# Optimization experiments

Measured on AMD Instinct MI355X. Metric: run time of the kernel, lower is better.

The kernel has to match this reference:

```python
import jax, jax.numpy as jnp
import numpy as np

N_FEATURES = 256
N_LAYERS = 256  # MZI layers; 2*N_LAYERS PSBS sublayers
BATCH = 1024


def _make_indexAB(nF):
    A = np.array([[2 * k, 2 * k + 1] for k in range(nF // 2)], np.int32)
    B = [[2 * k + 1, 2 * k + 2] for k in range((nF - 1) // 2)]
    while len(B) < nF // 2:
        B.append([-1, -1])  # padding sentinel, masked out
    return A, np.array(B, np.int32)


def _make_index(nF, nLayers):
    A, B = _make_indexAB(nF)
    blocks = ([A] * 2 + [B] * 2) * (nLayers // 2)
    if nLayers % 2 == 1:
        blocks += [A] * 2
    return np.stack(blocks).astype(np.int32)  # [2*nLayers, nF//2, 2]


def setup_inputs() -> dict:
    key = jax.random.key(0)
    k1, k2, k3 = jax.random.split(key, 3)
    nSub = 2 * N_LAYERS
    nAng = N_FEATURES // 2
    index = jnp.asarray(_make_index(N_FEATURES, N_LAYERS))
    return {
        "x_real": jax.random.normal(k1, (BATCH, N_FEATURES), jnp.float32),
        "x_imag": jax.random.normal(k2, (BATCH, N_FEATURES), jnp.float32),
        "params": jax.random.normal(k3, (nSub, nAng), jnp.float32),  # torch.randn init
        "ps_params": jnp.zeros((N_FEATURES,), jnp.float32),  # ModulePS zeros init
        "index": index,
        "split": jnp.zeros((nSub, nAng), jnp.float32),  # buffer, default zeros
        "atten": jnp.ones((nSub, N_FEATURES), jnp.float32),  # buffer, default ones
    }


def _psbs_mesh(x, params, i_safe, j_safe, valid, split, atten):
    # x: [B, F] complex64. Each sublayer: phase e^{i theta} on top port, then
    # beamsplitter [[cos a, i sin a],[i sin a, cos a]] with a = pi/4 + split,
    # then per-feature diagonal attenuation.
    def step(x, xs):
        theta, isf, jsf, vld, sp, at = xs
        xu = x[:, isf]  # [B, A]
        xv = x[:, jsf]
        u = xu * jnp.exp(1j * theta)[None, :]
        ang = jnp.float32(np.pi / 4) + sp
        t = jnp.cos(ang)
        r = jnp.sin(ang)
        yu = t * u + 1j * r * xv
        yv = 1j * r * u + t * xv
        zero = jnp.zeros((), x.dtype)
        # scatter deltas; invalid (padded) pairs add 0 so duplicate dummy index 0 is safe
        x = x.at[:, isf].add(jnp.where(vld, yu - xu, zero))
        x = x.at[:, jsf].add(jnp.where(vld, yv - xv, zero))
        return x * at[None, :], None

    x, _ = jax.lax.scan(step, x, (params, i_safe, j_safe, valid, split, atten))
    return x


def reference(x_real, x_imag, params, ps_params, index, split, atten):
    x = (x_real + 1j * x_imag).astype(jnp.complex64)
    i_idx = index[:, :, 0]
    j_idx = index[:, :, 1]
    valid = i_idx >= 0
    i_safe = jnp.where(valid, i_idx, 0)
    j_safe = jnp.where(valid, j_idx, 0)
    x = _psbs_mesh(x, params, i_safe, j_safe, valid, split, atten)
    # final diagonal phase shift (ModulePS)
    return x * jnp.exp(1j * ps_params)[None, :]
```

## Files before the change

kernel.cpp:

```cpp
#include <hip/hip_runtime.h>
#include <math.h>

#define NF    256
#define NSUB  512
#define NB    1024
#define NITER 128
#define PI4   0.78539816339744830962f

#define PS_OFF   (NITER * 1024)
#define FLAG_OFF (PS_OFF + 512)
#define WS_REQ   ((size_t)(FLAG_OFF + 1) * sizeof(float))

__device__ __forceinline__ bool looks_zero(const void* p) {
  const unsigned* u = (const unsigned*)p;
  return (u[1] | u[25] | u[111]) == 0u;
}
__device__ __forceinline__ bool looks_ones(const void* p) {
  const unsigned* u = (const unsigned*)p;
  return u[1] == 0x3F800000u && u[3] == 0x3F800000u && u[257] == 0x3F800000u;
}

__global__ void flag_init_kernel(float* ws) {
  ((unsigned*)ws)[FLAG_OFF] = 0u;
}

__global__ __launch_bounds__(256) void check_kernel(
    const void* __restrict__ pp0, const void* __restrict__ pp1,
    const void* __restrict__ pi0, const void* __restrict__ pi1,
    float* __restrict__ ws) {
  const unsigned* split = (const unsigned*)(looks_zero(pp0) ? pp0 : pp1);
  const unsigned* atten = (const unsigned*)(looks_ones(pi0) ? pi0 : pi1);
  const int i = blockIdx.x * 256 + threadIdx.x;
  unsigned bad = 0u;
  if (atten[i] != 0x3F800000u) bad = 1u;
  if (i < 65536 && split[i] != 0u) bad = 1u;
  if (bad) atomicOr(((unsigned*)ws) + FLAG_OFF, 1u);
}

__global__ __launch_bounds__(256) void precompute3_kernel(
    const void* __restrict__ pp0, const void* __restrict__ pp1,
    const float* __restrict__ psp, float* __restrict__ ws) {
  const float* params = looks_zero(pp0) ? (const float*)pp1 : (const float*)pp0;
  const int t = blockIdx.x;
  const int j = threadIdx.x;
  if (t == NITER) {
    float sn, cs;
    sincosf(psp[j], &sn, &cs);
    ((float2*)(ws + PS_OFF))[j] = make_float2(cs, sn);
    return;
  }
  float e1r, e1i, fr, fi;
  int k, ln;
  if (j < 128) {
    float s1, c1, s2, c2;
    sincosf(params[(size_t)(4 * t) * 128 + j], &s1, &c1);
    sincosf(params[(size_t)(4 * t + 1) * 128 + j], &s2, &c2);
    e1r = 0.5f * c1; e1i = 0.5f * s1;
    fr = 0.5f * (c2 + 1.f); fi = 0.5f * s2;
    k = j & 1; ln = j >> 1;
  } else {
    const int m = j - 128;
    if (m < 127) {
      float s1, c1, s2, c2;
      sincosf(params[(size_t)(4 * t + 2) * 128 + m], &s1, &c1);
      sincosf(params[(size_t)(4 * t + 3) * 128 + m], &s2, &c2);
      e1r = 0.5f * c1; e1i = 0.5f * s1;
      fr = 0.5f * (c2 + 1.f); fi = 0.5f * s2;
    } else {
      e1r = -0.5f; e1i = 0.f; fr = 0.f; fi = 0.f;
    }
    k = 2 + (m & 1); ln = m >> 1;
  }
  ((float4*)ws)[t * 256 + k * 64 + ln] = make_float4(e1r, e1i, fr, fi);
}

__device__ __forceinline__ void applyC(float& ur, float& ui, float& vr, float& vi,
                                       const float4 K) {
  const float wr = K.x * ur - K.y * ui;
  const float wi = K.x * ui + K.y * ur;
  const float e2r = 2.f * K.z - 1.f;
  const float e2i = 2.f * K.w;
  const float zr = e2r * wr - e2i * wi;
  const float zi = e2r * wi + e2i * wr;
  const float gr = K.z * vr - K.w * vi;
  const float gi = K.z * vi + K.w * vr;
  const float nur = (zr - wr) - gi;
  const float nui = (zi - wi) + gr;
  const float nvr = (vr - gr) - (zi + wi);
  const float nvi = (vi - gi) + (zr + wr);
  ur = nur; ui = nui; vr = nvr; vi = nvi;
}

__device__ __forceinline__ void mzi(float& ur, float& ui, float& vr, float& vi,
                                    const float4 k) {
  const float c = k.x, s = k.y, t = k.z, r = k.w;
  const float pr  = c * ur - s * ui;
  const float pi_ = s * ur + c * ui;
  const float nur = t * pr  - r * vi;
  const float nui = t * pi_ + r * vr;
  const float nvr = t * vr - r * pi_;
  const float nvi = t * vi + r * pr;
  ur = nur; ui = nui; vr = nvr; vi = nvi;
}
struct Coef { float4 a, b, c; };
__device__ __forceinline__ Coef makeCoefRaw(const float* params, const float* split,
                                            const float* atten, int s, int lane) {
  Coef k;
  const float2 th = *(const float2*)(params + (size_t)s * 128 + 2 * lane);
  const float2 sp = *(const float2*)(split + (size_t)s * 128 + 2 * lane);
  k.c = *(const float4*)(atten + (size_t)s * NF + 4 * lane);
  float sn, cs, rr, tt;
  sincosf(th.x, &sn, &cs);
  sincosf(PI4 + sp.x, &rr, &tt);
  k.a = make_float4(cs, sn, tt, rr);
  sincosf(th.y, &sn, &cs);
  sincosf(PI4 + sp.y, &rr, &tt);
  k.b = make_float4(cs, sn, tt, rr);
  return k;
}

#define ITER_BODY(C0, C1, C2, C3)                                          \
  {                                                                        \
    applyC(x0r, x0i, x1r, x1i, C0);                                        \
    applyC(x2r, x2i, x3r, x3i, C1);                                        \
    const float s0r = x0r, s0i = x0i;                                      \
    const float d3r = __shfl_down(x0r, 1), d3i = __shfl_down(x0i, 1);      \
    x0r = x1r; x0i = x1i; x1r = x2r; x1i = x2i; x2r = x3r; x2i = x3i;      \
    x3r = d3r; x3i = d3i;                                                  \
    applyC(x0r, x0i, x1r, x1i, C2);                                        \
    applyC(x2r, x2i, x3r, x3i, C3);                                        \
    const float u0r = __shfl_up(x3r, 1), u0i = __shfl_up(x3i, 1);          \
    x3r = x2r; x3i = x2i; x2r = x1r; x2i = x1i; x1r = x0r; x1i = x0i;      \
    x0r = lane ? u0r : s0r;                                                \
    x0i = lane ? u0i : s0i;                                                \
  }

__global__ __launch_bounds__(256) void mesh3_kernel(
    const float* __restrict__ xr_in, const float* __restrict__ xi_in,
    const float* __restrict__ ws,
    const void* __restrict__ pp0, const void* __restrict__ pp1,
    const void* __restrict__ pi0, const void* __restrict__ pi1,
    const float* __restrict__ psp,
    float* __restrict__ out) {
  const int lane = threadIdx.x & 63;
  const int wv   = threadIdx.x >> 6;
  const int row  = blockIdx.x * 4 + wv;

  const float4 r4 = ((const float4*)(xr_in + (size_t)row * NF))[lane];
  const float4 i4 = ((const float4*)(xi_in + (size_t)row * NF))[lane];
  float x0r = r4.x, x1r = r4.y, x2r = r4.z, x3r = r4.w;
  float x0i = i4.x, x1i = i4.y, x2i = i4.z, x3i = i4.w;

  const unsigned flag = ((const unsigned*)ws)[FLAG_OFF];
  if (flag == 0u) {
    const float4* cb = (const float4*)ws + lane;
    float4 A0 = cb[0],   A1 = cb[64],  A2 = cb[128], A3 = cb[192];
    float4 B0 = cb[256], B1 = cb[320], B2 = cb[384], B3 = cb[448];
#pragma unroll 1
    for (int tt = 0; tt < 64; ++tt) {
      const int pa = (tt < 63) ? (2 * tt + 2) * 256 : 0;
      const float4 nA0 = cb[pa], nA1 = cb[pa + 64], nA2 = cb[pa + 128], nA3 = cb[pa + 192];
      ITER_BODY(A0, A1, A2, A3);
      A0 = nA0; A1 = nA1; A2 = nA2; A3 = nA3;
      const int pb = (tt < 63) ? (2 * tt + 3) * 256 : 256;
      const float4 nB0 = cb[pb], nB1 = cb[pb + 64], nB2 = cb[pb + 128], nB3 = cb[pb + 192];
      ITER_BODY(B0, B1, B2, B3);
      B0 = nB0; B1 = nB1; B2 = nB2; B3 = nB3;
    }
    const float2* psc = (const float2*)(ws + PS_OFF);
    const float2 p0 = psc[4 * lane + 0];
    const float2 p1 = psc[4 * lane + 1];
    const float2 p2 = psc[4 * lane + 2];
    const float2 p3 = psc[4 * lane + 3];
    const float o0r = x0r * p0.x - x0i * p0.y, o0i = x0r * p0.y + x0i * p0.x;
    const float o1r = x1r * p1.x - x1i * p1.y, o1i = x1r * p1.y + x1i * p1.x;
    const float o2r = x2r * p2.x - x2i * p2.y, o2i = x2r * p2.y + x2i * p2.x;
    const float o3r = x3r * p3.x - x3i * p3.y, o3i = x3r * p3.y + x3i * p3.x;
    float4* op = (float4*)out;
    const size_t base = (size_t)row * 64 + lane;
    op[base] = make_float4(o0r, o1r, o2r, o3r);
    op[(size_t)NB * 64 + base] = make_float4(o0i, o1i, o2i, o3i);
    return;
  }

  {
    const float* params = looks_zero(pp0) ? (const float*)pp1 : (const float*)pp0;
    const float* split  = looks_zero(pp0) ? (const float*)pp0 : (const float*)pp1;
    const float* atten  = looks_ones(pi0) ? (const float*)pi0 : (const float*)pi1;
#pragma unroll 1
    for (int s = 0; s < NSUB; s += 4) {
      {
        Coef k = makeCoefRaw(params, split, atten, s, lane);
        mzi(x0r, x0i, x1r, x1i, k.a);
        mzi(x2r, x2i, x3r, x3i, k.b);
        x0r *= k.c.x; x0i *= k.c.x; x1r *= k.c.y; x1i *= k.c.y;
        x2r *= k.c.z; x2i *= k.c.z; x3r *= k.c.w; x3i *= k.c.w;
      }
      {
        Coef k = makeCoefRaw(params, split, atten, s + 1, lane);
        mzi(x0r, x0i, x1r, x1i, k.a);
        mzi(x2r, x2i, x3r, x3i, k.b);
        x0r *= k.c.x; x0i *= k.c.x; x1r *= k.c.y; x1i *= k.c.y;
        x2r *= k.c.z; x2i *= k.c.z; x3r *= k.c.w; x3i *= k.c.w;
      }
#pragma unroll
      for (int q = 2; q < 4; ++q) {
        Coef k = makeCoefRaw(params, split, atten, s + q, lane);
        mzi(x1r, x1i, x2r, x2i, k.a);
        const float nvr = __shfl_down(x0r, 1);
        const float nvi = __shfl_down(x0i, 1);
        const float c = k.b.x, sv = k.b.y, t = k.b.z, r = k.b.w;
        const float pr  = c * x3r - sv * x3i;
        const float pi_ = sv * x3r + c * x3i;
        const float yur = t * pr  - r * nvi;
        const float yui = t * pi_ + r * nvr;
        const float yvr = t * nvr - r * pi_;
        const float yvi = t * nvi + r * pr;
        const float svr = __shfl_up(yvr, 1);
        const float svi = __shfl_up(yvi, 1);
        if (lane < 63) { x3r = yur; x3i = yui; }
        if (lane > 0)  { x0r = svr; x0i = svi; }
        x0r *= k.c.x; x0i *= k.c.x; x1r *= k.c.y; x1i *= k.c.y;
        x2r *= k.c.z; x2i *= k.c.z; x3r *= k.c.w; x3i *= k.c.w;
      }
    }
    float c0, s0, c1, s1, c2, s2, c3, s3;
    sincosf(psp[4 * lane + 0], &s0, &c0);
    sincosf(psp[4 * lane + 1], &s1, &c1);
    sincosf(psp[4 * lane + 2], &s2, &c2);
    sincosf(psp[4 * lane + 3], &s3, &c3);
    const float o0r = x0r * c0 - x0i * s0, o0i = x0r * s0 + x0i * c0;
    const float o1r = x1r * c1 - x1i * s1, o1i = x1r * s1 + x1i * c1;
    const float o2r = x2r * c2 - x2i * s2, o2i = x2r * s2 + x2i * c2;
    const float o3r = x3r * c3 - x3i * s3, o3i = x3r * s3 + x3i * c3;
    float4* op = (float4*)out;
    const size_t base = (size_t)row * 64 + lane;
    op[base] = make_float4(o0r, o1r, o2r, o3r);
    op[(size_t)NB * 64 + base] = make_float4(o0i, o1i, o2i, o3i);
  }
}

__global__ __launch_bounds__(256) void mesh_raw_kernel(
    const float* __restrict__ xr_in, const float* __restrict__ xi_in,
    const void* __restrict__ pp0, const void* __restrict__ pp1,
    const void* __restrict__ pi0, const void* __restrict__ pi1,
    const float* __restrict__ psp, float* __restrict__ out) {
  const int lane = threadIdx.x & 63;
  const int wv   = threadIdx.x >> 6;
  const int row  = blockIdx.x * 4 + wv;
  const float4 r4 = ((const float4*)(xr_in + (size_t)row * NF))[lane];
  const float4 i4 = ((const float4*)(xi_in + (size_t)row * NF))[lane];
  float x0r = r4.x, x1r = r4.y, x2r = r4.z, x3r = r4.w;
  float x0i = i4.x, x1i = i4.y, x2i = i4.z, x3i = i4.w;
  const float* params = looks_zero(pp0) ? (const float*)pp1 : (const float*)pp0;
  const float* split  = looks_zero(pp0) ? (const float*)pp0 : (const float*)pp1;
  const float* atten  = looks_ones(pi0) ? (const float*)pi0 : (const float*)pi1;
#pragma unroll 1
  for (int s = 0; s < NSUB; s += 4) {
    for (int q = 0; q < 2; ++q) {
      Coef k = makeCoefRaw(params, split, atten, s + q, lane);
      mzi(x0r, x0i, x1r, x1i, k.a);
      mzi(x2r, x2i, x3r, x3i, k.b);
      x0r *= k.c.x; x0i *= k.c.x; x1r *= k.c.y; x1i *= k.c.y;
      x2r *= k.c.z; x2i *= k.c.z; x3r *= k.c.w; x3i *= k.c.w;
    }
    for (int q = 2; q < 4; ++q) {
      Coef k = makeCoefRaw(params, split, atten, s + q, lane);
      mzi(x1r, x1i, x2r, x2i, k.a);
      const float nvr = __shfl_down(x0r, 1);
      const float nvi = __shfl_down(x0i, 1);
      const float c = k.b.x, sv = k.b.y, t = k.b.z, r = k.b.w;
      const float pr  = c * x3r - sv * x3i;
      const float pi_ = sv * x3r + c * x3i;
      const float yur = t * pr  - r * nvi;
      const float yui = t * pi_ + r * nvr;
      const float yvr = t * nvr - r * pi_;
      const float yvi = t * nvi + r * pr;
      const float svr = __shfl_up(yvr, 1);
      const float svi = __shfl_up(yvi, 1);
      if (lane < 63) { x3r = yur; x3i = yui; }
      if (lane > 0)  { x0r = svr; x0i = svi; }
      x0r *= k.c.x; x0i *= k.c.x; x1r *= k.c.y; x1i *= k.c.y;
      x2r *= k.c.z; x2i *= k.c.z; x3r *= k.c.w; x3i *= k.c.w;
    }
  }
  float c0, s0, c1, s1, c2, s2, c3, s3;
  sincosf(psp[4 * lane + 0], &s0, &c0);
  sincosf(psp[4 * lane + 1], &s1, &c1);
  sincosf(psp[4 * lane + 2], &s2, &c2);
  sincosf(psp[4 * lane + 3], &s3, &c3);
  const float o0r = x0r * c0 - x0i * s0, o0i = x0r * s0 + x0i * c0;
  const float o1r = x1r * c1 - x1i * s1, o1i = x1r * s1 + x1i * c1;
  const float o2r = x2r * c2 - x2i * s2, o2i = x2r * s2 + x2i * c2;
  const float o3r = x3r * c3 - x3i * s3, o3i = x3r * s3 + x3i * c3;
  float4* op = (float4*)out;
  const size_t base = (size_t)row * 64 + lane;
  op[base] = make_float4(o0r, o1r, o2r, o3r);
  op[(size_t)NB * 64 + base] = make_float4(o0i, o1i, o2i, o3i);
}

extern "C" void kernel_launch(void* const* d_in, const int* in_sizes, int n_in,
                              void* d_out, int out_size, void* d_ws, size_t ws_size,
                              hipStream_t stream) {
  const void* px[2] = { d_in[0], d_in[1] };
  const void* pp[2] = { d_in[2], d_in[5] };
  const void* pi2[2] = { d_in[4], d_in[6] };
  const void* pps = d_in[3];
  {
    const void* sx[2]; const void* sp[2]; const void* si[2];
    const void* s256 = nullptr;
    int nx = 0, npp = 0, ni = 0;
    for (int i = 0; i < n_in; ++i) {
      const int sz = in_sizes[i];
      if (sz == 262144 && nx < 2)      sx[nx++] = d_in[i];
      else if (sz == 65536 && npp < 2) sp[npp++] = d_in[i];
      else if (sz == 131072 && ni < 2) si[ni++] = d_in[i];
      else if (sz == 256)              s256 = d_in[i];
    }
    if (nx == 2)  { px[0] = sx[0];  px[1] = sx[1]; }
    if (npp == 2) { pp[0] = sp[0];  pp[1] = sp[1]; }
    if (ni == 2)  { pi2[0] = si[0]; pi2[1] = si[1]; }
    if (s256)     pps = s256;
  }
  float* out = (float*)d_out;

  if (ws_size >= WS_REQ) {
    float* ws = (float*)d_ws;
    flag_init_kernel<<<1, 1, 0, stream>>>(ws);
    check_kernel<<<512, 256, 0, stream>>>(pp[0], pp[1], pi2[0], pi2[1], ws);
    precompute3_kernel<<<NITER + 1, 256, 0, stream>>>(pp[0], pp[1],
                                                      (const float*)pps, ws);
    mesh3_kernel<<<NB / 4, 256, 0, stream>>>(
        (const float*)px[0], (const float*)px[1], ws,
        pp[0], pp[1], pi2[0], pi2[1], (const float*)pps, out);
  } else {
    mesh_raw_kernel<<<NB / 4, 256, 0, stream>>>(
        (const float*)px[0], (const float*)px[1],
        pp[0], pp[1], pi2[0], pi2[1], (const float*)pps, out);
  }
}
```

Before: 64.87 us.

## Collapse groups of eight sublayers into banded 9-tap transfer kernels

Adds a precompute that multiplies every 8 consecutive PSBS sublayers into a banded 9-diagonal complex transfer matrix per output feature. The mesh kernel then applies 64 banded mat-vec steps using neighbour shuffles, instead of 512 sublayer updates. This cuts the serial dependency chain and the number of shuffles per row. In exchange it adds a memset, two precompute kernels and more coefficient loads per step, and the fallback raw path moves into a separate guarded kernel. The fast path still depends on the existing check that split is zero and atten is one.

```diff
diff --git a/kernel.cpp b/kernel.cpp
--- a/kernel.cpp
+++ b/kernel.cpp
@@ -5,11 +5,17 @@
 #define NSUB  512
 #define NB    1024
 #define NITER 128
+#define NGRP  64
 #define PI4   0.78539816339744830962f
+#define RS    0.70710678118654752440f
 
 #define PS_OFF   (NITER * 1024)
 #define FLAG_OFF (PS_OFF + 512)
-#define WS_REQ   ((size_t)(FLAG_OFF + 1) * sizeof(float))
+#define KB_OFF   131600
+#define KB_FLOATS (NGRP * 9 * 256 * 2)
+#define E_OFF    (KB_OFF + KB_FLOATS)
+#define WS1_REQ  ((size_t)(FLAG_OFF + 1) * sizeof(float))
+#define WS2_REQ  ((size_t)(E_OFF + NSUB * 128 * 2) * sizeof(float))
 
 __device__ __forceinline__ bool looks_zero(const void* p) {
   const unsigned* u = (const unsigned*)p;
@@ -74,6 +80,149 @@
   ((float4*)ws)[t * 256 + k * 64 + ln] = make_float4(e1r, e1i, fr, fi);
 }
 
+__global__ __launch_bounds__(128) void stage1_kernel(
+    const void* __restrict__ pp0, const void* __restrict__ pp1,
+    float* __restrict__ ws) {
+  const float* params = looks_zero(pp0) ? (const float*)pp1 : (const float*)pp0;
+  const int idx = blockIdx.x * 128 + threadIdx.x;
+  float sn, cs;
+  sincosf(params[idx], &sn, &cs);
+  ws[E_OFF + 2 * idx]     = cs;
+  ws[E_OFF + 2 * idx + 1] = sn;
+}
+
+__global__ __launch_bounds__(256) void stage2_kernel(float* __restrict__ ws) {
+  const int g = blockIdx.x;
+  const int j = threadIdx.x;
+  const float2* Et = (const float2*)(ws + E_OFF);
+  float wr[9], wi[9];
+#pragma unroll
+  for (int q = 0; q < 9; ++q) { wr[q] = 0.f; wi[q] = 0.f; }
+  wr[4] = 1.f;
+  const bool jeven = ((j & 1) == 0);
+
+#define FULLPAIR(SU)                                                        \
+  {                                                                         \
+    const int p = j - 4 + (SU);                                             \
+    const bool ok = isA ? (p >= 0 && p <= 254) : (p >= 1 && p <= 253);      \
+    if (ok) {                                                               \
+      const float2 E = Et[s * 128 + (isA ? (p >> 1) : ((p - 1) >> 1))];     \
+      const float ur = wr[SU], ui = wi[SU];                                 \
+      const float vr = wr[(SU) + 1], vi = wi[(SU) + 1];                     \
+      const float er = E.x * ur - E.y * ui;                                 \
+      const float ei = E.x * ui + E.y * ur;                                 \
+      wr[SU] = (er - vi) * RS;       wi[SU] = (ei + vr) * RS;               \
+      wr[(SU) + 1] = (vr - ei) * RS; wi[(SU) + 1] = (vi + er) * RS;         \
+    }                                                                       \
+  }
+#define HALFU8                                                              \
+  {                                                                         \
+    const int p = j + 4;                                                    \
+    const bool ok = isA ? (p >= 0 && p <= 254) : (p >= 1 && p <= 253);      \
+    if (ok) {                                                               \
+      const float2 E = Et[s * 128 + (isA ? (p >> 1) : ((p - 1) >> 1))];     \
+      const float er = E.x * wr[8] - E.y * wi[8];                           \
+      const float ei = E.x * wi[8] + E.y * wr[8];                           \
+      wr[8] = er * RS; wi[8] = ei * RS;                                     \
+    }                                                                       \
+  }
+#define HALFV0                                                              \
+  {                                                                         \
+    const int p = j - 5;                                                    \
+    const bool ok = isA ? (p >= 0) : (p >= 1);                              \
+    if (ok) { wr[0] *= RS; wi[0] *= RS; }                                   \
+  }
+
+#pragma unroll
+  for (int ss = 0; ss < 8; ++ss) {
+    const int s = 8 * g + ss;
+    const bool isA = ((ss & 2) == 0);
+    const bool pat0 = (jeven == isA);
+    if (pat0) {
+      FULLPAIR(0) FULLPAIR(2) FULLPAIR(4) FULLPAIR(6) HALFU8
+    } else {
+      FULLPAIR(1) FULLPAIR(3) FULLPAIR(5) FULLPAIR(7) HALFV0
+    }
+  }
+#undef FULLPAIR
+#undef HALFU8
+#undef HALFV0
+
+#pragma unroll
+  for (int slot = 0; slot < 9; ++slot) {
+    const int f = j - 4 + slot;
+    if (f >= 0 && f < 256) {
+      const size_t o = KB_OFF + (((size_t)g * 9 + (8 - slot)) * 256 + f) * 2;
+      ws[o]     = wr[slot];
+      ws[o + 1] = wi[slot];
+    }
+  }
+}
+
+__global__ __launch_bounds__(256) void mesh6_kernel(
+    const float* __restrict__ xr_in, const float* __restrict__ xi_in,
+    const float* __restrict__ ws, float* __restrict__ out) {
+  if (((const unsigned*)ws)[FLAG_OFF] != 0u) return;
+  const int lane = threadIdx.x & 63;
+  const int wv   = threadIdx.x >> 6;
+  const int row  = blockIdx.x * 4 + wv;
+
+  const float4 r4 = ((const float4*)(xr_in + (size_t)row * NF))[lane];
+  const float4 i4 = ((const float4*)(xi_in + (size_t)row * NF))[lane];
+  float x0r = r4.x, x1r = r4.y, x2r = r4.z, x3r = r4.w;
+  float x0i = i4.x, x1i = i4.y, x2i = i4.z, x3i = i4.w;
+
+  const float* kb = ws + KB_OFF + 8 * lane;
+
+#pragma unroll 1
+  for (int g = 0; g < NGRP; ++g) {
+    float xwr[12], xwi[12];
+    xwr[0] = __shfl_up(x0r, 1);  xwi[0] = __shfl_up(x0i, 1);
+    xwr[1] = __shfl_up(x1r, 1);  xwi[1] = __shfl_up(x1i, 1);
+    xwr[2] = __shfl_up(x2r, 1);  xwi[2] = __shfl_up(x2i, 1);
+    xwr[3] = __shfl_up(x3r, 1);  xwi[3] = __shfl_up(x3i, 1);
+    xwr[4] = x0r; xwi[4] = x0i;  xwr[5] = x1r; xwi[5] = x1i;
+    xwr[6] = x2r; xwi[6] = x2i;  xwr[7] = x3r; xwi[7] = x3i;
+    xwr[8]  = __shfl_down(x0r, 1); xwi[8]  = __shfl_down(x0i, 1);
+    xwr[9]  = __shfl_down(x1r, 1); xwi[9]  = __shfl_down(x1i, 1);
+    xwr[10] = __shfl_down(x2r, 1); xwi[10] = __shfl_down(x2i, 1);
+    xwr[11] = __shfl_down(x3r, 1); xwi[11] = __shfl_down(x3i, 1);
+
+    float ar0 = 0.f, ai0 = 0.f, ar1 = 0.f, ai1 = 0.f;
+    float ar2 = 0.f, ai2 = 0.f, ar3 = 0.f, ai3 = 0.f;
+    const float* kg = kb + (size_t)g * 4608;
+#pragma unroll
+    for (int dd = 0; dd < 9; ++dd) {
+      const float4 ka = *(const float4*)(kg + dd * 512);
+      const float4 kc = *(const float4*)(kg + dd * 512 + 4);
+      ar0 = fmaf(ka.x, xwr[dd], ar0);     ar0 = fmaf(-ka.y, xwi[dd], ar0);
+      ai0 = fmaf(ka.x, xwi[dd], ai0);     ai0 = fmaf(ka.y, xwr[dd], ai0);
+      ar1 = fmaf(ka.z, xwr[dd + 1], ar1); ar1 = fmaf(-ka.w, xwi[dd + 1], ar1);
+      ai1 = fmaf(ka.z, xwi[dd + 1], ai1); ai1 = fmaf(ka.w, xwr[dd + 1], ai1);
+      ar2 = fmaf(kc.x, xwr[dd + 2], ar2); ar2 = fmaf(-kc.y, xwi[dd + 2], ar2);
+      ai2 = fmaf(kc.x, xwi[dd + 2], ai2); ai2 = fmaf(kc.y, xwr[dd + 2], ai2);
+      ar3 = fmaf(kc.z, xwr[dd + 3], ar3); ar3 = fmaf(-kc.w, xwi[dd + 3], ar3);
+      ai3 = fmaf(kc.z, xwi[dd + 3], ai3); ai3 = fmaf(kc.w, xwr[dd + 3], ai3);
+    }
+    x0r = ar0; x0i = ai0; x1r = ar1; x1i = ai1;
+    x2r = ar2; x2i = ai2; x3r = ar3; x3i = ai3;
+  }
+
+  const float2* psc = (const float2*)(ws + PS_OFF);
+  const float2 p0 = psc[4 * lane + 0];
+  const float2 p1 = psc[4 * lane + 1];
+  const float2 p2 = psc[4 * lane + 2];
+  const float2 p3 = psc[4 * lane + 3];
+  const float o0r = x0r * p0.x - x0i * p0.y, o0i = x0r * p0.y + x0i * p0.x;
+  const float o1r = x1r * p1.x - x1i * p1.y, o1i = x1r * p1.y + x1i * p1.x;
+  const float o2r = x2r * p2.x - x2i * p2.y, o2i = x2r * p2.y + x2i * p2.x;
+  const float o3r = x3r * p3.x - x3i * p3.y, o3i = x3r * p3.y + x3i * p3.x;
+  float4* op = (float4*)out;
+  const size_t base = (size_t)row * 64 + lane;
+  op[base] = make_float4(o0r, o1r, o2r, o3r);
+  op[(size_t)NB * 64 + base] = make_float4(o0i, o1i, o2i, o3i);
+}
+
 __device__ __forceinline__ void applyC(float& ur, float& ui, float& vr, float& vi,
                                        const float4 K) {
   const float wr = K.x * ur - K.y * ui;
@@ -91,6 +240,62 @@
   ur = nur; ui = nui; vr = nvr; vi = nvi;
 }
 
+#define ITER_BODY(C0, C1, C2, C3)                                          \
+  {                                                                        \
+    applyC(x0r, x0i, x1r, x1i, C0);                                        \
+    applyC(x2r, x2i, x3r, x3i, C1);                                        \
+    const float s0r = x0r, s0i = x0i;                                      \
+    const float d3r = __shfl_down(x0r, 1), d3i = __shfl_down(x0i, 1);      \
+    x0r = x1r; x0i = x1i; x1r = x2r; x1i = x2i; x2r = x3r; x2i = x3i;      \
+    x3r = d3r; x3i = d3i;                                                  \
+    applyC(x0r, x0i, x1r, x1i, C2);                                        \
+    applyC(x2r, x2i, x3r, x3i, C3);                                        \
+    const float u0r = __shfl_up(x3r, 1), u0i = __shfl_up(x3i, 1);          \
+    x3r = x2r; x3i = x2i; x2r = x1r; x2i = x1i; x1r = x0r; x1i = x0i;      \
+    x0r = lane ? u0r : s0r;                                                \
+    x0i = lane ? u0i : s0i;                                                \
+  }
+
+__global__ __launch_bounds__(256) void mesh3_kernel(
+    const float* __restrict__ xr_in, const float* __restrict__ xi_in,
+    const float* __restrict__ ws, float* __restrict__ out) {
+  if (((const unsigned*)ws)[FLAG_OFF] != 0u) return;
+  const int lane = threadIdx.x & 63;
+  const int wv   = threadIdx.x >> 6;
+  const int row  = blockIdx.x * 4 + wv;
+  const float4 r4 = ((const float4*)(xr_in + (size_t)row * NF))[lane];
+  const float4 i4 = ((const float4*)(xi_in + (size_t)row * NF))[lane];
+  float x0r = r4.x, x1r = r4.y, x2r = r4.z, x3r = r4.w;
+  float x0i = i4.x, x1i = i4.y, x2i = i4.z, x3i = i4.w;
+  const float4* cb = (const float4*)ws + lane;
+  float4 A0 = cb[0],   A1 = cb[64],  A2 = cb[128], A3 = cb[192];
+  float4 B0 = cb[256], B1 = cb[320], B2 = cb[384], B3 = cb[448];
+#pragma unroll 1
+  for (int tt = 0; tt < 64; ++tt) {
+    const int pa = (tt < 63) ? (2 * tt + 2) * 256 : 0;
+    const float4 nA0 = cb[pa], nA1 = cb[pa + 64], nA2 = cb[pa + 128], nA3 = cb[pa + 192];
+    ITER_BODY(A0, A1, A2, A3);
+    A0 = nA0; A1 = nA1; A2 = nA2; A3 = nA3;
+    const int pb = (tt < 63) ? (2 * tt + 3) * 256 : 256;
+    const float4 nB0 = cb[pb], nB1 = cb[pb + 64], nB2 = cb[pb + 128], nB3 = cb[pb + 192];
+    ITER_BODY(B0, B1, B2, B3);
+    B0 = nB0; B1 = nB1; B2 = nB2; B3 = nB3;
+  }
+  const float2* psc = (const float2*)(ws + PS_OFF);
+  const float2 p0 = psc[4 * lane + 0];
+  const float2 p1 = psc[4 * lane + 1];
+  const float2 p2 = psc[4 * lane + 2];
+  const float2 p3 = psc[4 * lane + 3];
+  const float o0r = x0r * p0.x - x0i * p0.y, o0i = x0r * p0.y + x0i * p0.x;
+  const float o1r = x1r * p1.x - x1i * p1.y, o1i = x1r * p1.y + x1i * p1.x;
+  const float o2r = x2r * p2.x - x2i * p2.y, o2i = x2r * p2.y + x2i * p2.x;
+  const float o3r = x3r * p3.x - x3i * p3.y, o3i = x3r * p3.y + x3i * p3.x;
+  float4* op = (float4*)out;
+  const size_t base = (size_t)row * 64 + lane;
+  op[base] = make_float4(o0r, o1r, o2r, o3r);
+  op[(size_t)NB * 64 + base] = make_float4(o0i, o1i, o2i, o3i);
+}
+
 __device__ __forceinline__ void mzi(float& ur, float& ui, float& vr, float& vi,
                                     const float4 k) {
   const float c = k.x, s = k.y, t = k.z, r = k.w;
@@ -119,132 +324,14 @@
   return k;
 }
 
-#define ITER_BODY(C0, C1, C2, C3)                                          \
-  {                                                                        \
-    applyC(x0r, x0i, x1r, x1i, C0);                                        \
-    applyC(x2r, x2i, x3r, x3i, C1);                                        \
-    const float s0r = x0r, s0i = x0i;                                      \
-    const float d3r = __shfl_down(x0r, 1), d3i = __shfl_down(x0i, 1);      \
-    x0r = x1r; x0i = x1i; x1r = x2r; x1i = x2i; x2r = x3r; x2i = x3i;      \
-    x3r = d3r; x3i = d3i;                                                  \
-    applyC(x0r, x0i, x1r, x1i, C2);                                        \
-    applyC(x2r, x2i, x3r, x3i, C3);                                        \
-    const float u0r = __shfl_up(x3r, 1), u0i = __shfl_up(x3i, 1);          \
-    x3r = x2r; x3i = x2i; x2r = x1r; x2i = x1i; x1r = x0r; x1i = x0i;      \
-    x0r = lane ? u0r : s0r;                                                \
-    x0i = lane ? u0i : s0i;                                                \
-  }
-
-__global__ __launch_bounds__(256) void mesh3_kernel(
-    const float* __restrict__ xr_in, const float* __restrict__ xi_in,
-    const float* __restrict__ ws,
-    const void* __restrict__ pp0, const void* __restrict__ pp1,
-    const void* __restrict__ pi0, const void* __restrict__ pi1,
-    const float* __restrict__ psp,
-    float* __restrict__ out) {
-  const int lane = threadIdx.x & 63;
-  const int wv   = threadIdx.x >> 6;
-  const int row  = blockIdx.x * 4 + wv;
-
-  const float4 r4 = ((const float4*)(xr_in + (size_t)row * NF))[lane];
-  const float4 i4 = ((const float4*)(xi_in + (size_t)row * NF))[lane];
-  float x0r = r4.x, x1r = r4.y, x2r = r4.z, x3r = r4.w;
-  float x0i = i4.x, x1i = i4.y, x2i = i4.z, x3i = i4.w;
-
-  const unsigned flag = ((const unsigned*)ws)[FLAG_OFF];
-  if (flag == 0u) {
-    const float4* cb = (const float4*)ws + lane;
-    float4 A0 = cb[0],   A1 = cb[64],  A2 = cb[128], A3 = cb[192];
-    float4 B0 = cb[256], B1 = cb[320], B2 = cb[384], B3 = cb[448];
-#pragma unroll 1
-    for (int tt = 0; tt < 64; ++tt) {
-      const int pa = (tt < 63) ? (2 * tt + 2) * 256 : 0;
-      const float4 nA0 = cb[pa], nA1 = cb[pa + 64], nA2 = cb[pa + 128], nA3 = cb[pa + 192];
-      ITER_BODY(A0, A1, A2, A3);
-      A0 = nA0; A1 = nA1; A2 = nA2; A3 = nA3;
-      const int pb = (tt < 63) ? (2 * tt + 3) * 256 : 256;
-      const float4 nB0 = cb[pb], nB1 = cb[pb + 64], nB2 = cb[pb + 128], nB3 = cb[pb + 192];
-      ITER_BODY(B0, B1, B2, B3);
-      B0 = nB0; B1 = nB1; B2 = nB2; B3 = nB3;
-    }
-    const float2* psc = (const float2*)(ws + PS_OFF);
-    const float2 p0 = psc[4 * lane + 0];
-    const float2 p1 = psc[4 * lane + 1];
-    const float2 p2 = psc[4 * lane + 2];
-    const float2 p3 = psc[4 * lane + 3];
-    const float o0r = x0r * p0.x - x0i * p0.y, o0i = x0r * p0.y + x0i * p0.x;
-    const float o1r = x1r * p1.x - x1i * p1.y, o1i = x1r * p1.y + x1i * p1.x;
-    const float o2r = x2r * p2.x - x2i * p2.y, o2i = x2r * p2.y + x2i * p2.x;
-    const float o3r = x3r * p3.x - x3i * p3.y, o3i = x3r * p3.y + x3i * p3.x;
-    float4* op = (float4*)out;
-    const size_t base = (size_t)row * 64 + lane;
-    op[base] = make_float4(o0r, o1r, o2r, o3r);
-    op[(size_t)NB * 64 + base] = make_float4(o0i, o1i, o2i, o3i);
-    return;
-  }
-
-  {
-    const float* params = looks_zero(pp0) ? (const float*)pp1 : (const float*)pp0;
-    const float* split  = looks_zero(pp0) ? (const float*)pp0 : (const float*)pp1;
-    const float* atten  = looks_ones(pi0) ? (const float*)pi0 : (const float*)pi1;
-#pragma unroll 1
-    for (int s = 0; s < NSUB; s += 4) {
-      {
-        Coef k = makeCoefRaw(params, split, atten, s, lane);
-        mzi(x0r, x0i, x1r, x1i, k.a);
-        mzi(x2r, x2i, x3r, x3i, k.b);
-        x0r *= k.c.x; x0i *= k.c.x; x1r *= k.c.y; x1i *= k.c.y;
-        x2r *= k.c.z; x2i *= k.c.z; x3r *= k.c.w; x3i *= k.c.w;
-      }
-      {
-        Coef k = makeCoefRaw(params, split, atten, s + 1, lane);
-        mzi(x0r, x0i, x1r, x1i, k.a);
-        mzi(x2r, x2i, x3r, x3i, k.b);
-        x0r *= k.c.x; x0i *= k.c.x; x1r *= k.c.y; x1i *= k.c.y;
-        x2r *= k.c.z; x2i *= k.c.z; x3r *= k.c.w; x3i *= k.c.w;
-      }
-#pragma unroll
-      for (int q = 2; q < 4; ++q) {
-        Coef k = makeCoefRaw(params, split, atten, s + q, lane);
-        mzi(x1r, x1i, x2r, x2i, k.a);
-        const float nvr = __shfl_down(x0r, 1);
-        const float nvi = __shfl_down(x0i, 1);
-        const float c = k.b.x, sv = k.b.y, t = k.b.z, r = k.b.w;
-        const float pr  = c * x3r - sv * x3i;
-        const float pi_ = sv * x3r + c * x3i;
-        const float yur = t * pr  - r * nvi;
-        const float yui = t * pi_ + r * nvr;
-        const float yvr = t * nvr - r * pi_;
-        const float yvi = t * nvi + r * pr;
-        const float svr = __shfl_up(yvr, 1);
-        const float svi = __shfl_up(yvi, 1);
-        if (lane < 63) { x3r = yur; x3i = yui; }
-        if (lane > 0)  { x0r = svr; x0i = svi; }
-        x0r *= k.c.x; x0i *= k.c.x; x1r *= k.c.y; x1i *= k.c.y;
-        x2r *= k.c.z; x2i *= k.c.z; x3r *= k.c.w; x3i *= k.c.w;
-      }
-    }
-    float c0, s0, c1, s1, c2, s2, c3, s3;
-    sincosf(psp[4 * lane + 0], &s0, &c0);
-    sincosf(psp[4 * lane + 1], &s1, &c1);
-    sincosf(psp[4 * lane + 2], &s2, &c2);
-    sincosf(psp[4 * lane + 3], &s3, &c3);
-    const float o0r = x0r * c0 - x0i * s0, o0i = x0r * s0 + x0i * c0;
-    const float o1r = x1r * c1 - x1i * s1, o1i = x1r * s1 + x1i * c1;
-    const float o2r = x2r * c2 - x2i * s2, o2i = x2r * s2 + x2i * c2;
-    const float o3r = x3r * c3 - x3i * s3, o3i = x3r * s3 + x3i * c3;
-    float4* op = (float4*)out;
-    const size_t base = (size_t)row * 64 + lane;
-    op[base] = make_float4(o0r, o1r, o2r, o3r);
-    op[(size_t)NB * 64 + base] = make_float4(o0i, o1i, o2i, o3i);
-  }
-}
-
+template <bool GUARDED>
 __global__ __launch_bounds__(256) void mesh_raw_kernel(
     const float* __restrict__ xr_in, const float* __restrict__ xi_in,
     const void* __restrict__ pp0, const void* __restrict__ pp1,
     const void* __restrict__ pi0, const void* __restrict__ pi1,
-    const float* __restrict__ psp, float* __restrict__ out) {
+    const float* __restrict__ psp, const float* __restrict__ ws,
+    float* __restrict__ out) {
+  if (GUARDED && ((const unsigned*)ws)[FLAG_OFF] == 0u) return;
   const int lane = threadIdx.x & 63;
   const int wv   = threadIdx.x >> 6;
   const int row  = blockIdx.x * 4 + wv;
@@ -324,18 +411,35 @@
   }
   float* out = (float*)d_out;
 
-  if (ws_size >= WS_REQ) {
+  if (ws_size >= WS2_REQ) {
+    float* ws = (float*)d_ws;
+    flag_init_kernel<<<1, 1, 0, stream>>>(ws);
+    check_kernel<<<512, 256, 0, stream>>>(pp[0], pp[1], pi2[0], pi2[1], ws);
+    precompute3_kernel<<<NITER + 1, 256, 0, stream>>>(pp[0], pp[1],
+                                                      (const float*)pps, ws);
+    hipMemsetAsync((char*)d_ws + (size_t)KB_OFF * 4, 0,
+                   (size_t)KB_FLOATS * 4, stream);
+    stage1_kernel<<<NSUB, 128, 0, stream>>>(pp[0], pp[1], ws);
+    stage2_kernel<<<NGRP, 256, 0, stream>>>(ws);
+    mesh6_kernel<<<NB / 4, 256, 0, stream>>>(
+        (const float*)px[0], (const float*)px[1], ws, out);
+    mesh_raw_kernel<true><<<NB / 4, 256, 0, stream>>>(
+        (const float*)px[0], (const float*)px[1],
+        pp[0], pp[1], pi2[0], pi2[1], (const float*)pps, ws, out);
+  } else if (ws_size >= WS1_REQ) {
     float* ws = (float*)d_ws;
     flag_init_kernel<<<1, 1, 0, stream>>>(ws);
     check_kernel<<<512, 256, 0, stream>>>(pp[0], pp[1], pi2[0], pi2[1], ws);
     precompute3_kernel<<<NITER + 1, 256, 0, stream>>>(pp[0], pp[1],
                                                       (const float*)pps, ws);
     mesh3_kernel<<<NB / 4, 256, 0, stream>>>(
-        (const float*)px[0], (const float*)px[1], ws,
-        pp[0], pp[1], pi2[0], pi2[1], (const float*)pps, out);
+        (const float*)px[0], (const float*)px[1], ws, out);
+    mesh_raw_kernel<true><<<NB / 4, 256, 0, stream>>>(
+        (const float*)px[0], (const float*)px[1],
+        pp[0], pp[1], pi2[0], pi2[1], (const float*)pps, ws, out);
   } else {
-    mesh_raw_kernel<<<NB / 4, 256, 0, stream>>>(
+    mesh_raw_kernel<false><<<NB / 4, 256, 0, stream>>>(
         (const float*)px[0], (const float*)px[1],
-        pp[0], pp[1], pi2[0], pi2[1], (const float*)pps, out);
-  }
-}
+        pp[0], pp[1], pi2[0], pi2[1], (const float*)pps, nullptr, out);
+  }
+}
```

Result: slower. 174.5 us (+169.0%).
